# Optimization experiments

Hardware: AMD Instinct MI355X
Metric: run time of the kernel (lower is better)

Reference implementation:

```python
import jax, jax.numpy as jnp
import numpy as np

H = 256; NH = 4; DH = H // NH
NT, NS, NV = 4096, 2048, 1024
E1, E2, E3 = 65536, 16384, 32768
LN_EPS = 1e-5


def setup_inputs() -> dict:
    key = jax.random.key(0)
    ks = jax.random.split(key, 40)
    def nrm(i, shape):
        return jax.random.normal(ks[i], shape, jnp.float32) * 0.05
    inp = {
        "x_term": jax.random.normal(ks[0], (NT, H), jnp.float32),
        "x_symbol": jax.random.normal(ks[1], (NS, H), jnp.float32),
        "x_var": jax.random.normal(ks[2], (NV, H), jnp.float32),
        "ha_src": jax.random.randint(ks[3], (E1,), 0, NT),
        "ha_dst": jax.random.randint(ks[4], (E1,), 0, NT),
        "so_src": jax.random.randint(ks[5], (E2,), 0, NT),
        "so_dst": jax.random.randint(ks[6], (E2,), 0, NS),
        "vo_src": jax.random.randint(ks[7], (E3,), 0, NV),
        "vo_dst": jax.random.randint(ks[8], (E3,), 0, NT),
        # SAGEConv params for the 4 term-destination relations
        "Wl_rha": nrm(9, (H, H)),  "bl_rha": nrm(10, (H,)), "Wr_rha": nrm(11, (H, H)),
        "Wl_ha":  nrm(12, (H, H)), "bl_ha":  nrm(13, (H,)), "Wr_ha":  nrm(14, (H, H)),
        "Wl_rsym": nrm(15, (H, H)), "bl_rsym": nrm(16, (H,)), "Wr_rsym": nrm(17, (H, H)),
        "Wl_var": nrm(18, (H, H)), "bl_var": nrm(19, (H,)), "Wr_var": nrm(20, (H, H)),
        "ln_g": jnp.ones((H,), jnp.float32),
        "ln_b": jnp.zeros((H,), jnp.float32),
        "in_proj_w": nrm(21, (3 * H, H)),
        "in_proj_b": nrm(22, (3 * H,)),
        "out_proj_w": nrm(23, (H, H)),
        "out_proj_b": nrm(24, (H,)),
        "post_w": nrm(25, (H, H)),
        "post_b": nrm(26, (H,)),
    }
    return inp


def _sage(x_src, x_dst, src, dst, Wl, bl, Wr, num_dst):
    # PyG SAGEConv: lin_l(mean_j x_src[j]) + lin_r(x_dst)
    msg = x_src[src]                                            # [E, H] gather
    s = jax.ops.segment_sum(msg, dst, num_segments=num_dst)     # [N_dst, H] scatter-add
    cnt = jax.ops.segment_sum(jnp.ones((src.shape[0],), x_src.dtype), dst,
                              num_segments=num_dst)
    agg = s / jnp.maximum(cnt, 1.0)[:, None]
    return agg @ Wl.T + bl + x_dst @ Wr.T


def _layernorm(x, g, b):
    mu = jnp.mean(x, axis=-1, keepdims=True)
    var = jnp.mean(jnp.square(x - mu), axis=-1, keepdims=True)
    return (x - mu) * jax.lax.rsqrt(var + LN_EPS) * g + b


def _mha(x, in_w, in_b, out_w, out_b):
    # torch MultiheadAttention (eval, batch=1, self-attention)
    qkv = x @ in_w.T + in_b                       # [N, 3H]
    q, k, v = jnp.split(qkv, 3, axis=-1)
    def heads(t):
        return t.reshape(-1, NH, DH).transpose(1, 0, 2)  # [NH, N, DH]
    q, k, v = heads(q), heads(k), heads(v)
    scores = jnp.einsum("hqd,hkd->hqk", q, k) / np.sqrt(DH).astype(np.float32)
    a = jax.nn.softmax(scores, axis=-1)
    o = jnp.einsum("hqk,hkd->hqd", a, v)          # [NH, N, DH]
    o = o.transpose(1, 0, 2).reshape(-1, H)
    return o @ out_w.T + out_b


def reference(x_term, x_symbol, x_var,
              ha_src, ha_dst, so_src, so_dst, vo_src, vo_dst,
              Wl_rha, bl_rha, Wr_rha, Wl_ha, bl_ha, Wr_ha,
              Wl_rsym, bl_rsym, Wr_rsym, Wl_var, bl_var, Wr_var,
              ln_g, ln_b, in_proj_w, in_proj_b, out_proj_w, out_proj_b,
              post_w, post_b):
    nt = x_term.shape[0]
    # HeteroConv(aggr='sum') over the 4 relations whose destination is 'term'
    conv_term = (
        _sage(x_term, x_term, ha_dst, ha_src, Wl_rha, bl_rha, Wr_rha, nt)    # rev_has_arg
        + _sage(x_term, x_term, ha_src, ha_dst, Wl_ha, bl_ha, Wr_ha, nt)     # has_arg
        + _sage(x_symbol, x_term, so_dst, so_src, Wl_rsym, bl_rsym, Wr_rsym, nt)  # rev_symbol_of
        + _sage(x_var, x_term, vo_src, vo_dst, Wl_var, bl_var, Wr_var, nt)   # var_occurrence
    )
    term_out = _layernorm(conv_term + x_term, ln_g, ln_b)  # dropout is identity in eval
    attn_out = _mha(term_out, in_proj_w, in_proj_b, out_proj_w, out_proj_b)
    post = jax.nn.relu(attn_out @ post_w.T + post_b)
    term_final = post + term_out
    return term_final
```

## Files before the change

kernel.cpp:

```cpp
#include <hip/hip_runtime.h>
#include <hip/hip_bf16.h>

#define H 256
#define NT 4096
#define NHEAD 4
#define E1 65536
#define E2 16384
#define E3 32768
#define TOTE (2 * E1 + E2 + E3)
#define LN_EPS 1e-5f
#define SPLIT 4

typedef __hip_bfloat16 bf16;
typedef short bf16x8 __attribute__((ext_vector_type(8)));
typedef float f32x4 __attribute__((ext_vector_type(4)));

__device__ __forceinline__ float b2f(bf16 v) { return __bfloat162float(v); }
__device__ __forceinline__ float u2f(unsigned short u) {
    unsigned int x = ((unsigned int)u) << 16;
    return __uint_as_float(x);
}
__device__ __forceinline__ unsigned short f2u(float f) {
    bf16 h = __float2bfloat16(f);
    unsigned short v;
    __builtin_memcpy(&v, &h, 2);
    return v;
}
__device__ __forceinline__ float ldin(const void* p, size_t i, bool isbf) {
    return isbf ? b2f(((const bf16*)p)[i]) : ((const float*)p)[i];
}

__global__ __launch_bounds__(256) void k_init(float4* cnt4, int n4,
                                              const unsigned int* __restrict__ lng,
                                              unsigned int* __restrict__ flag) {
    int i = blockIdx.x * 256 + threadIdx.x;
    if (i == 0) *flag = (lng[0] == 0x3F803F80u) ? 1u : 0u;
    int stride = gridDim.x * 256;
    float4 z = make_float4(0.f, 0.f, 0.f, 0.f);
    for (; i < n4; i += stride) cnt4[i] = z;
}

__global__ __launch_bounds__(256) void k_count4(const int* __restrict__ s0, const int* __restrict__ s1,
                                                const int* __restrict__ s2, const int* __restrict__ s3,
                                                int* __restrict__ cnt) {
    int i = blockIdx.x * 256 + threadIdx.x;
    int r, e;
    if (i < E1) { r = 0; e = i; }
    else if (i < 2 * E1) { r = 1; e = i - E1; }
    else if (i < 2 * E1 + E2) { r = 2; e = i - 2 * E1; }
    else if (i < TOTE) { r = 3; e = i - 2 * E1 - E2; }
    else return;
    const int* s = (r == 0) ? s0 : (r == 1) ? s1 : (r == 2) ? s2 : s3;
    atomicAdd(&cnt[r * NT + s[e]], 1);
}

__global__ __launch_bounds__(256) void k_scan(const int* __restrict__ cnt, int* __restrict__ offs,
                                              int* __restrict__ cursor) {
    __shared__ int tot[256];
    int t = threadIdx.x, r = blockIdx.x;
    const int* c = cnt + r * NT;
    int* o = offs + r * (NT + 1);
    int* cur = cursor + r * NT;
    int base = t * 16;
    int local[16];
    int sum = 0;
#pragma unroll
    for (int j = 0; j < 16; j++) { local[j] = c[base + j]; sum += local[j]; }
    tot[t] = sum;
    __syncthreads();
    if (t == 0) {
        int run = 0;
        for (int i = 0; i < 256; i++) { int v = tot[i]; tot[i] = run; run += v; }
        o[NT] = run;
    }
    __syncthreads();
    int run = tot[t];
#pragma unroll
    for (int j = 0; j < 16; j++) { o[base + j] = run; cur[base + j] = run; run += local[j]; }
}

__global__ __launch_bounds__(256) void k_fill(const int* __restrict__ s0, const int* __restrict__ s1,
                                              const int* __restrict__ s2, const int* __restrict__ s3,
                                              const int* __restrict__ g0, const int* __restrict__ g1,
                                              const int* __restrict__ g2, const int* __restrict__ g3,
                                              int* __restrict__ cursor, int* __restrict__ csr) {
    int i = blockIdx.x * 256 + threadIdx.x;
    int r, e, rb;
    if (i < E1) { r = 0; e = i; rb = 0; }
    else if (i < 2 * E1) { r = 1; e = i - E1; rb = E1; }
    else if (i < 2 * E1 + E2) { r = 2; e = i - 2 * E1; rb = 2 * E1; }
    else if (i < TOTE) { r = 3; e = i - 2 * E1 - E2; rb = 2 * E1 + E2; }
    else return;
    const int* s = (r == 0) ? s0 : (r == 1) ? s1 : (r == 2) ? s2 : s3;
    const int* g = (r == 0) ? g0 : (r == 1) ? g1 : (r == 2) ? g2 : g3;
    int d = s[e];
    int pos = atomicAdd(&cursor[r * NT + d], 1);
    csr[rb + pos] = g[e];
}

__global__ __launch_bounds__(256) void k_gatherA(
    const void* __restrict__ x0, const void* __restrict__ x1,
    const void* __restrict__ x2, const void* __restrict__ x3,
    const int* __restrict__ offs, const int* __restrict__ csr,
    bf16* __restrict__ aggs, const unsigned int* __restrict__ flag) {
    int y = blockIdx.y;
    int i = blockIdx.x * 4 + (threadIdx.x >> 6);
    int lane = threadIdx.x & 63;
    bool isbf = (*flag != 0u);
    const void* x = (y == 0) ? x0 : (y == 1) ? x1 : (y == 2) ? x2 : x3;
    static const int rbase[4] = {0, E1, 2 * E1, 2 * E1 + E2};
    const int* o = offs + y * (NT + 1);
    const int* cs = csr + rbase[y];
    int b = o[i], e = o[i + 1];
    float ax = 0.f, ay = 0.f, az = 0.f, aw = 0.f;
    if (isbf) {
        for (int j = b; j < e; j++) {
            int s = cs[j];
            ushort4 u = *(const ushort4*)((const unsigned short*)x + (size_t)s * H + lane * 4);
            ax += u2f(u.x); ay += u2f(u.y); az += u2f(u.z); aw += u2f(u.w);
        }
    } else {
        for (int j = b; j < e; j++) {
            int s = cs[j];
            float4 v = *(const float4*)((const float*)x + (size_t)s * H + lane * 4);
            ax += v.x; ay += v.y; az += v.z; aw += v.w;
        }
    }
    float inv = 1.0f / fmaxf((float)(e - b), 1.0f);
    *(ushort4*)((unsigned short*)aggs + ((size_t)y * NT + i) * H + lane * 4) =
        make_ushort4(f2u(ax * inv), f2u(ay * inv), f2u(az * inv), f2u(aw * inv));
}

__global__ __launch_bounds__(256) void k_prepB(
    const void* __restrict__ Wl0, const void* __restrict__ Wl1,
    const void* __restrict__ Wl2, const void* __restrict__ Wl3,
    const void* __restrict__ Wr0, const void* __restrict__ Wr1,
    const void* __restrict__ Wr2, const void* __restrict__ Wr3,
    const void* __restrict__ b0, const void* __restrict__ b1,
    const void* __restrict__ b2, const void* __restrict__ b3,
    bf16* __restrict__ Bcat, float* __restrict__ bsum, const unsigned int* __restrict__ flag) {
    int idx = blockIdx.x * 256 + threadIdx.x;
    bool isbf = (*flag != 0u);
    int n = idx / 1280, k = idx % 1280;
    float v;
    if (k < 1024) {
        const void* W = (k < 256) ? Wl0 : (k < 512) ? Wl1 : (k < 768) ? Wl2 : Wl3;
        v = ldin(W, (size_t)n * 256 + (k & 255), isbf);
    } else {
        size_t o = (size_t)n * 256 + (k - 1024);
        v = ldin(Wr0, o, isbf) + ldin(Wr1, o, isbf) + ldin(Wr2, o, isbf) + ldin(Wr3, o, isbf);
    }
    ((unsigned short*)Bcat)[idx] = f2u(v);
    if (idx < 256)
        bsum[idx] = ldin(b0, idx, isbf) + ldin(b1, idx, isbf) + ldin(b2, idx, isbf) + ldin(b3, idx, isbf);
}

__global__ __launch_bounds__(256) void k_convln(
    const bf16* __restrict__ aggs, const bf16* __restrict__ Bcat, const float* __restrict__ bsum,
    const void* __restrict__ xt, const void* __restrict__ gw, const void* __restrict__ gb,
    bf16* __restrict__ term, const unsigned int* __restrict__ flag) {
    __shared__ unsigned short Asm[4 * 16 * 8];
    __shared__ unsigned short Bsm[4 * 256 * 8];
    __shared__ float redS[4][16];
    const bool isbf = (*flag != 0u);
    const int tid = threadIdx.x;
    const int w = tid >> 6, lane = tid & 63;
    const int col = lane & 15, quad = lane >> 4;
    const int m0 = blockIdx.x * 16;
    const int srow = tid & 63, skq = tid >> 6;

    f32x4 acc[4];
#pragma unroll
    for (int dt = 0; dt < 4; dt++) acc[dt] = (f32x4){0.f, 0.f, 0.f, 0.f};

    bf16x8 areg;
    bf16x8 breg[4];
    auto loadA = [&](int k0) {
        if (tid < 64) {
            int row = tid & 15, akq = tid >> 4;
            int k = k0 + akq * 8;
            if (k < 1024) {
                areg = *(const bf16x8*)((const unsigned short*)aggs +
                                        ((size_t)(k >> 8) * NT + m0 + row) * 256 + (k & 255));
            } else {
#pragma unroll
                for (int j = 0; j < 8; j++)
                    areg[j] = (short)f2u(ldin(xt, (size_t)(m0 + row) * 256 + (k - 1024) + j, isbf));
            }
        }
    };
    auto loadB = [&](int k0) {
#pragma unroll
        for (int t = 0; t < 4; t++)
            breg[t] = *(const bf16x8*)((const unsigned short*)Bcat +
                                       (size_t)(t * 64 + srow) * 1280 + k0 + skq * 8);
    };

    loadA(0);
    loadB(0);
    for (int k0 = 0; k0 < 1280; k0 += 32) {
        __syncthreads();
        if (tid < 64) *(bf16x8*)&Asm[tid * 8] = areg;
#pragma unroll
        for (int t = 0; t < 4; t++)
            *(bf16x8*)&Bsm[(skq * 256 + t * 64 + srow) * 8] = breg[t];
        __syncthreads();
        if (k0 + 32 < 1280) { loadA(k0 + 32); loadB(k0 + 32); }
        bf16x8 a = *(const bf16x8*)&Asm[(quad * 16 + col) * 8];
#pragma unroll
        for (int dt = 0; dt < 4; dt++) {
            bf16x8 b = *(const bf16x8*)&Bsm[(quad * 256 + w * 64 + dt * 16 + col) * 8];
            acc[dt] = __builtin_amdgcn_mfma_f32_16x16x32_bf16(a, b, acc[dt], 0, 0, 0);
        }
    }

#pragma unroll
    for (int dt = 0; dt < 4; dt++) {
        int n = w * 64 + dt * 16 + col;
        float bsv = bsum[n];
#pragma unroll
        for (int r = 0; r < 4; r++) {
            int m = m0 + quad * 4 + r;
            acc[dt][r] += bsv + ldin(xt, (size_t)m * 256 + n, isbf);
        }
    }
    float mu[4], rs_[4];
#pragma unroll
    for (int r = 0; r < 4; r++) {
        float s = acc[0][r] + acc[1][r] + acc[2][r] + acc[3][r];
#pragma unroll
        for (int mk = 1; mk <= 8; mk <<= 1) s += __shfl_xor(s, mk);
        if (col == 0) redS[w][quad * 4 + r] = s;
    }
    __syncthreads();
#pragma unroll
    for (int r = 0; r < 4; r++) {
        int m = quad * 4 + r;
        mu[r] = (redS[0][m] + redS[1][m] + redS[2][m] + redS[3][m]) * (1.0f / 256.0f);
    }
    __syncthreads();
#pragma unroll
    for (int r = 0; r < 4; r++) {
        float s2 = 0.f;
#pragma unroll
        for (int dt = 0; dt < 4; dt++) {
            float d = acc[dt][r] - mu[r];
            s2 += d * d;
        }
#pragma unroll
        for (int mk = 1; mk <= 8; mk <<= 1) s2 += __shfl_xor(s2, mk);
        if (col == 0) redS[w][quad * 4 + r] = s2;
    }
    __syncthreads();
#pragma unroll
    for (int r = 0; r < 4; r++) {
        int m = quad * 4 + r;
        float var = (redS[0][m] + redS[1][m] + redS[2][m] + redS[3][m]) * (1.0f / 256.0f);
        rs_[r] = rsqrtf(var + LN_EPS);
    }
#pragma unroll
    for (int dt = 0; dt < 4; dt++) {
        int n = w * 64 + dt * 16 + col;
        float gv = ldin(gw, n, isbf), bv = ldin(gb, n, isbf);
#pragma unroll
        for (int r = 0; r < 4; r++) {
            int m = m0 + quad * 4 + r;
            term[(size_t)m * 256 + n] = __float2bfloat16((acc[dt][r] - mu[r]) * rs_[r] * gv + bv);
        }
    }
}

template <int AMODE, int EPI>
__global__ __launch_bounds__(256) void k_gemm(
    const void* __restrict__ A, const void* __restrict__ A2, const float* __restrict__ ml,
    const void* __restrict__ B, const void* __restrict__ bias,
    const bf16* __restrict__ resid, void* __restrict__ outp,
    int M, int N, int K, const unsigned int* __restrict__ flag) {
    __shared__ unsigned short Asm[4 * 64 * 8];
    __shared__ unsigned short Bsm[4 * 64 * 8];
    const bool isbf = (*flag != 0u);
    const int tid = threadIdx.x;
    const int w = tid >> 6, lane = tid & 63;
    const int col = lane & 15, quad = lane >> 4;
    const int m0 = blockIdx.x * 64, n0 = blockIdx.y * 64;
    const int srow = tid & 63, skq = tid >> 6;
    const int am = m0 + srow;

    f32x4 acc[4];
#pragma unroll
    for (int dt = 0; dt < 4; dt++) acc[dt] = (f32x4){0.f, 0.f, 0.f, 0.f};

    bf16x8 areg, breg;
    auto loadA = [&](int k0) {
        int k = k0 + skq * 8;
        if (AMODE == 0) {
            areg = *(const bf16x8*)((const unsigned short*)A + (size_t)am * K + k);
        } else {
            int h = k >> 6;
            float l0 = ml[(size_t)(0 * NHEAD + h) * NT + am];
            float l1 = ml[(size_t)(1 * NHEAD + h) * NT + am];
            float l2 = ml[(size_t)(2 * NHEAD + h) * NT + am];
            float l3 = ml[(size_t)(3 * NHEAD + h) * NT + am];
            float iw = 1.0f / (l0 + l1 + l2 + l3);
            bf16x8 o0 = *(const bf16x8*)((const unsigned short*)A + (size_t)am * H + k);
            bf16x8 o1 = *(const bf16x8*)((const unsigned short*)A + ((size_t)NT + am) * H + k);
            bf16x8 o2 = *(const bf16x8*)((const unsigned short*)A2 + (size_t)am * H + k);
            bf16x8 o3 = *(const bf16x8*)((const unsigned short*)A2 + ((size_t)NT + am) * H + k);
#pragma unroll
            for (int j = 0; j < 8; j++)
                areg[j] = (short)f2u((l0 * u2f((unsigned short)o0[j]) + l1 * u2f((unsigned short)o1[j]) +
                                      l2 * u2f((unsigned short)o2[j]) + l3 * u2f((unsigned short)o3[j])) * iw);
        }
    };
    auto loadB = [&](int k0) {
        size_t bi = (size_t)(n0 + srow) * K + k0 + skq * 8;
        if (isbf) {
            breg = *(const bf16x8*)((const unsigned short*)B + bi);
        } else {
#pragma unroll
            for (int j = 0; j < 8; j++) breg[j] = (short)f2u(((const float*)B)[bi + j]);
        }
    };

    loadA(0);
    loadB(0);
    for (int k0 = 0; k0 < K; k0 += 32) {
        __syncthreads();
        *(bf16x8*)&Asm[tid * 8] = areg;
        *(bf16x8*)&Bsm[tid * 8] = breg;
        __syncthreads();
        if (k0 + 32 < K) { loadA(k0 + 32); loadB(k0 + 32); }
        bf16x8 a = *(const bf16x8*)&Asm[(quad * 64 + w * 16 + col) * 8];
#pragma unroll
        for (int dt = 0; dt < 4; dt++) {
            bf16x8 b = *(const bf16x8*)&Bsm[(quad * 64 + dt * 16 + col) * 8];
            acc[dt] = __builtin_amdgcn_mfma_f32_16x16x32_bf16(a, b, acc[dt], 0, 0, 0);
        }
    }
#pragma unroll
    for (int dt = 0; dt < 4; dt++) {
        int n = n0 + dt * 16 + col;
        float bv = ldin(bias, n, isbf);
#pragma unroll
        for (int r = 0; r < 4; r++) {
            int m = m0 + w * 16 + quad * 4 + r;
            float v = acc[dt][r] + bv;
            size_t off = (size_t)m * N + n;
            if (EPI == 2) {
                v = fmaxf(v, 0.f);
                v += b2f(resid[off]);
                ((float*)outp)[off] = v;
            } else {
                ((bf16*)outp)[off] = __float2bfloat16(v);
            }
        }
    }
}

__global__ __launch_bounds__(256) void k_attn(const bf16* __restrict__ qkv,
                                              bf16* __restrict__ opart01,
                                              bf16* __restrict__ opart23,
                                              float* __restrict__ ml) {
    __shared__ unsigned short Ksm[8 * 64 * 8];
    __shared__ unsigned short Vt[8 * 64 * 8];
    __shared__ unsigned short Psm[4][1024];
    const int h = blockIdx.y, sp = blockIdx.z;
    const int q0 = blockIdx.x * 64;
    const int tid = threadIdx.x;
    const int w = tid >> 6, lane = tid & 63;
    const int col = lane & 15, quad = lane >> 4;
    const unsigned short* qk = (const unsigned short*)qkv;

    bf16x8 aQ[2];
#pragma unroll
    for (int ch = 0; ch < 2; ch++)
        aQ[ch] = *(const bf16x8*)(qk + (size_t)(q0 + w * 16 + col) * 768 + h * 64 + ch * 32 + quad * 8);

    f32x4 O[4];
#pragma unroll
    for (int dt = 0; dt < 4; dt++) O[dt] = (f32x4){0.f, 0.f, 0.f, 0.f};
    float lsum[4] = {0.f, 0.f, 0.f, 0.f};

    const int kbeg = sp * (NT / SPLIT), kend = kbeg + NT / SPLIT;
    const float SC = 0.125f * 1.44269504f;

    bf16x8 kreg[2], vreg[2];
    auto loadKV = [&](int kb) {
#pragma unroll
        for (int it = 0; it < 2; it++) {
            int cid = tid + it * 256;
            int kkey = cid & 63, dhq = cid >> 6;
            kreg[it] = *(const bf16x8*)(qk + (size_t)(kb + kkey) * 768 + 256 + h * 64 + dhq * 8);
            int vkey = cid >> 3, d8 = cid & 7;
            vreg[it] = *(const bf16x8*)(qk + (size_t)(kb + vkey) * 768 + 512 + h * 64 + d8 * 8);
        }
    };
    loadKV(kbeg);

    for (int kb = kbeg; kb < kend; kb += 64) {
        __syncthreads();
#pragma unroll
        for (int it = 0; it < 2; it++) {
            int cid = tid + it * 256;
            *(bf16x8*)&Ksm[cid * 8] = kreg[it];
            int vkey = cid >> 3, d8 = cid & 7;
            int kh = (vkey >> 3) * 512 + (vkey & 7);
#pragma unroll
            for (int jj = 0; jj < 8; jj++) {
                int j = (jj + lane) & 7;
                Vt[kh + (d8 * 8 + j) * 8] = (unsigned short)vreg[it][j];
            }
        }
        __syncthreads();
        if (kb + 64 < kend) loadKV(kb + 64);

        f32x4 c[4];
#pragma unroll
        for (int dt = 0; dt < 4; dt++) {
            c[dt] = (f32x4){0.f, 0.f, 0.f, 0.f};
#pragma unroll
            for (int ch = 0; ch < 2; ch++) {
                bf16x8 b = *(const bf16x8*)&Ksm[((ch * 4 + quad) * 64 + dt * 16 + col) * 8];
                c[dt] = __builtin_amdgcn_mfma_f32_16x16x32_bf16(aQ[ch], b, c[dt], 0, 0, 0);
            }
#pragma unroll
            for (int r = 0; r < 4; r++) {
                float p = exp2f(c[dt][r] * SC);
                c[dt][r] = p;
                lsum[r] += p;
            }
        }
#pragma unroll
        for (int dt = 0; dt < 4; dt++) {
            int k = dt * 16 + col;
#pragma unroll
            for (int r = 0; r < 4; r++) {
                int ql = quad * 4 + r;
                Psm[w][(k >> 3) * 128 + ql * 8 + (k & 7)] = f2u(c[dt][r]);
            }
        }
        bf16x8 aP[2];
#pragma unroll
        for (int kc = 0; kc < 2; kc++)
            aP[kc] = *(const bf16x8*)&Psm[w][(kc * 4 + quad) * 128 + col * 8];
#pragma unroll
        for (int dt = 0; dt < 4; dt++) {
#pragma unroll
            for (int kc = 0; kc < 2; kc++) {
                bf16x8 b = *(const bf16x8*)&Vt[((kc * 4 + quad) * 64 + dt * 16 + col) * 8];
                O[dt] = __builtin_amdgcn_mfma_f32_16x16x32_bf16(aP[kc], b, O[dt], 0, 0, 0);
            }
        }
    }
    float l[4];
#pragma unroll
    for (int r = 0; r < 4; r++) {
        float s = lsum[r];
#pragma unroll
        for (int mk = 1; mk <= 8; mk <<= 1) s += __shfl_xor(s, mk);
        l[r] = s;
    }
    bf16* ob = (sp < 2) ? (opart01 + (size_t)sp * NT * H) : (opart23 + (size_t)(sp - 2) * NT * H);
#pragma unroll
    for (int dt = 0; dt < 4; dt++) {
#pragma unroll
        for (int r = 0; r < 4; r++) {
            int q = q0 + w * 16 + quad * 4 + r;
            ob[(size_t)q * H + h * 64 + dt * 16 + col] = __float2bfloat16(O[dt][r] / l[r]);
        }
    }
    if (col == 0) {
#pragma unroll
        for (int r = 0; r < 4; r++) {
            int q = q0 + w * 16 + quad * 4 + r;
            ml[((size_t)sp * NHEAD + h) * NT + q] = l[r];
        }
    }
}

extern "C" void kernel_launch(void* const* d_in, const int* in_sizes, int n_in,
                              void* d_out, int out_size, void* d_ws, size_t ws_size,
                              hipStream_t stream) {
    const void* x_term   = d_in[0];
    const void* x_symbol = d_in[1];
    const void* x_var    = d_in[2];
    const int* ha_src = (const int*)d_in[3];
    const int* ha_dst = (const int*)d_in[4];
    const int* so_src = (const int*)d_in[5];
    const int* so_dst = (const int*)d_in[6];
    const int* vo_src = (const int*)d_in[7];
    const int* vo_dst = (const int*)d_in[8];
    const void* Wl[4]  = {d_in[9],  d_in[12], d_in[15], d_in[18]};
    const void* blv[4] = {d_in[10], d_in[13], d_in[16], d_in[19]};
    const void* Wr[4]  = {d_in[11], d_in[14], d_in[17], d_in[20]};
    const void* ln_g = d_in[21];
    const void* ln_b = d_in[22];
    const void* in_w = d_in[23];
    const void* in_b = d_in[24];
    const void* out_w = d_in[25];
    const void* out_b = d_in[26];
    const void* post_w = d_in[27];
    const void* post_b = d_in[28];

    char* ws = (char*)d_ws;
    unsigned int* flag = (unsigned int*)ws;
    char* csrbase = ws + 256;
    int* cnt    = (int*)csrbase;
    int* offs   = (int*)(csrbase + 65536);
    int* cursor = (int*)(csrbase + 132096);
    int* csr    = (int*)(csrbase + 197632);
    bf16*  Bcat = (bf16*)csrbase;
    float* bsum = (float*)(csrbase + 655360);
    float* ml   = (float*)csrbase;
    bf16* aggs  = (bf16*)(ws + (1 << 20));
    bf16* term  = (bf16*)(ws + (1 << 20) + 8388608);
    bf16* opart23 = (bf16*)(ws + (1 << 20) + 10485760);
    bf16* qkvp  = aggs;
    bf16* proj  = aggs;
    bf16* opart01 = (bf16*)d_out;

    k_init<<<16, 256, 0, stream>>>((float4*)cnt, 4 * NT / 4, (const unsigned int*)ln_g, flag);
    k_count4<<<(TOTE + 255) / 256, 256, 0, stream>>>(ha_src, ha_dst, so_src, vo_dst, cnt);
    k_scan<<<4, 256, 0, stream>>>(cnt, offs, cursor);
    k_fill<<<(TOTE + 255) / 256, 256, 0, stream>>>(ha_src, ha_dst, so_src, vo_dst,
                                                   ha_dst, ha_src, so_dst, vo_src, cursor, csr);
    k_gatherA<<<dim3(NT / 4, 4), 256, 0, stream>>>(x_term, x_term, x_symbol, x_var,
                                                   offs, csr, aggs, flag);
    k_prepB<<<(256 * 1280) / 256, 256, 0, stream>>>(Wl[0], Wl[1], Wl[2], Wl[3],
                                                    Wr[0], Wr[1], Wr[2], Wr[3],
                                                    blv[0], blv[1], blv[2], blv[3],
                                                    Bcat, bsum, flag);

    k_convln<<<256, 256, 0, stream>>>(aggs, Bcat, bsum, x_term, ln_g, ln_b, term, flag);

    k_gemm<0, 0><<<dim3(64, 12), 256, 0, stream>>>(
        term, nullptr, nullptr, in_w, in_b, nullptr, qkvp, NT, 768, 256, flag);

    k_attn<<<dim3(64, NHEAD, SPLIT), 256, 0, stream>>>(qkvp, opart01, opart23, ml);

    k_gemm<1, 0><<<dim3(64, 4), 256, 0, stream>>>(
        opart01, opart23, ml, out_w, out_b, nullptr, proj, NT, 256, 256, flag);

    k_gemm<0, 2><<<dim3(64, 4), 256, 0, stream>>>(
        proj, nullptr, nullptr, post_w, post_b, term, d_out, NT, 256, 256, flag);

    (void)in_sizes; (void)n_in; (void)out_size; (void)ws_size;
}
```

Measured before the change: 309.1 us.

## Write V transposed from QKV GEMM and drop attention LDS staging; fuse weight prep

The QKV projection epilogue now writes Q and K into a 512-wide buffer and writes V transposed into a separate buffer. The attention kernel can then load K and V MFMA operands straight from global memory into registers, removing the shared-memory staging, the in-LDS V transpose and the per-block barriers. Separately, the k_prepB weight-concatenation kernel is removed and convln reads and sums the SAGE weights and biases inline, saving a launch. The trade-off is repeated global or L2 loads per wave in attention, and redundant Wr summation across convln blocks.

```diff
diff --git a/kernel.cpp b/kernel.cpp
--- a/kernel.cpp
+++ b/kernel.cpp
@@ -131,32 +131,14 @@
         make_ushort4(f2u(ax * inv), f2u(ay * inv), f2u(az * inv), f2u(aw * inv));
 }
 
-__global__ __launch_bounds__(256) void k_prepB(
+__global__ __launch_bounds__(256) void k_convln(
+    const bf16* __restrict__ aggs,
     const void* __restrict__ Wl0, const void* __restrict__ Wl1,
     const void* __restrict__ Wl2, const void* __restrict__ Wl3,
     const void* __restrict__ Wr0, const void* __restrict__ Wr1,
     const void* __restrict__ Wr2, const void* __restrict__ Wr3,
-    const void* __restrict__ b0, const void* __restrict__ b1,
-    const void* __restrict__ b2, const void* __restrict__ b3,
-    bf16* __restrict__ Bcat, float* __restrict__ bsum, const unsigned int* __restrict__ flag) {
-    int idx = blockIdx.x * 256 + threadIdx.x;
-    bool isbf = (*flag != 0u);
-    int n = idx / 1280, k = idx % 1280;
-    float v;
-    if (k < 1024) {
-        const void* W = (k < 256) ? Wl0 : (k < 512) ? Wl1 : (k < 768) ? Wl2 : Wl3;
-        v = ldin(W, (size_t)n * 256 + (k & 255), isbf);
-    } else {
-        size_t o = (size_t)n * 256 + (k - 1024);
-        v = ldin(Wr0, o, isbf) + ldin(Wr1, o, isbf) + ldin(Wr2, o, isbf) + ldin(Wr3, o, isbf);
-    }
-    ((unsigned short*)Bcat)[idx] = f2u(v);
-    if (idx < 256)
-        bsum[idx] = ldin(b0, idx, isbf) + ldin(b1, idx, isbf) + ldin(b2, idx, isbf) + ldin(b3, idx, isbf);
-}
-
-__global__ __launch_bounds__(256) void k_convln(
-    const bf16* __restrict__ aggs, const bf16* __restrict__ Bcat, const float* __restrict__ bsum,
+    const void* __restrict__ bl0, const void* __restrict__ bl1,
+    const void* __restrict__ bl2, const void* __restrict__ bl3,
     const void* __restrict__ xt, const void* __restrict__ gw, const void* __restrict__ gb,
     bf16* __restrict__ term, const unsigned int* __restrict__ flag) {
     __shared__ unsigned short Asm[4 * 16 * 8];
@@ -190,10 +172,29 @@
         }
     };
     auto loadB = [&](int k0) {
-#pragma unroll
-        for (int t = 0; t < 4; t++)
-            breg[t] = *(const bf16x8*)((const unsigned short*)Bcat +
-                                       (size_t)(t * 64 + srow) * 1280 + k0 + skq * 8);
+        int k = k0 + skq * 8;
+#pragma unroll
+        for (int t = 0; t < 4; t++) {
+            int n = t * 64 + srow;
+            bf16x8 s;
+            if (k < 1024) {
+                const void* W = (k < 256) ? Wl0 : (k < 512) ? Wl1 : (k < 768) ? Wl2 : Wl3;
+                size_t o = (size_t)n * 256 + (k & 255);
+                if (isbf) {
+                    s = *(const bf16x8*)((const unsigned short*)W + o);
+                } else {
+#pragma unroll
+                    for (int j = 0; j < 8; j++) s[j] = (short)f2u(((const float*)W)[o + j]);
+                }
+            } else {
+                size_t o = (size_t)n * 256 + (k - 1024);
+#pragma unroll
+                for (int j = 0; j < 8; j++)
+                    s[j] = (short)f2u(ldin(Wr0, o + j, isbf) + ldin(Wr1, o + j, isbf) +
+                                      ldin(Wr2, o + j, isbf) + ldin(Wr3, o + j, isbf));
+            }
+            breg[t] = s;
+        }
     };
 
     loadA(0);
@@ -217,7 +218,7 @@
 #pragma unroll
     for (int dt = 0; dt < 4; dt++) {
         int n = w * 64 + dt * 16 + col;
-        float bsv = bsum[n];
+        float bsv = ldin(bl0, n, isbf) + ldin(bl1, n, isbf) + ldin(bl2, n, isbf) + ldin(bl3, n, isbf);
 #pragma unroll
         for (int r = 0; r < 4; r++) {
             int m = m0 + quad * 4 + r;
@@ -274,7 +275,7 @@
 __global__ __launch_bounds__(256) void k_gemm(
     const void* __restrict__ A, const void* __restrict__ A2, const float* __restrict__ ml,
     const void* __restrict__ B, const void* __restrict__ bias,
-    const bf16* __restrict__ resid, void* __restrict__ outp,
+    const bf16* __restrict__ resid, bf16* __restrict__ vt, void* __restrict__ outp,
     int M, int N, int K, const unsigned int* __restrict__ flag) {
     __shared__ unsigned short Asm[4 * 64 * 8];
     __shared__ unsigned short Bsm[4 * 64 * 8];
@@ -341,40 +342,49 @@
     for (int dt = 0; dt < 4; dt++) {
         int n = n0 + dt * 16 + col;
         float bv = ldin(bias, n, isbf);
+        if (EPI == 3 && n0 >= 512) {
+            int m = m0 + w * 16 + quad * 4;
+            *(ushort4*)((unsigned short*)vt + (size_t)(n - 512) * NT + m) =
+                make_ushort4(f2u(acc[dt][0] + bv), f2u(acc[dt][1] + bv),
+                             f2u(acc[dt][2] + bv), f2u(acc[dt][3] + bv));
+            continue;
+        }
 #pragma unroll
         for (int r = 0; r < 4; r++) {
             int m = m0 + w * 16 + quad * 4 + r;
             float v = acc[dt][r] + bv;
-            size_t off = (size_t)m * N + n;
-            if (EPI == 2) {
+            if (EPI == 3) {
+                ((bf16*)outp)[(size_t)m * 512 + n] = __float2bfloat16(v);
+            } else if (EPI == 2) {
+                size_t off = (size_t)m * N + n;
                 v = fmaxf(v, 0.f);
                 v += b2f(resid[off]);
                 ((float*)outp)[off] = v;
             } else {
-                ((bf16*)outp)[off] = __float2bfloat16(v);
+                ((bf16*)outp)[(size_t)m * N + n] = __float2bfloat16(v);
             }
         }
     }
 }
 
-__global__ __launch_bounds__(256) void k_attn(const bf16* __restrict__ qkv,
+__global__ __launch_bounds__(256) void k_attn(const bf16* __restrict__ qkvQK,
+                                              const bf16* __restrict__ vt,
                                               bf16* __restrict__ opart01,
                                               bf16* __restrict__ opart23,
                                               float* __restrict__ ml) {
-    __shared__ unsigned short Ksm[8 * 64 * 8];
-    __shared__ unsigned short Vt[8 * 64 * 8];
     __shared__ unsigned short Psm[4][1024];
     const int h = blockIdx.y, sp = blockIdx.z;
     const int q0 = blockIdx.x * 64;
     const int tid = threadIdx.x;
     const int w = tid >> 6, lane = tid & 63;
     const int col = lane & 15, quad = lane >> 4;
-    const unsigned short* qk = (const unsigned short*)qkv;
+    const unsigned short* qk = (const unsigned short*)qkvQK;
+    const unsigned short* vp = (const unsigned short*)vt;
 
     bf16x8 aQ[2];
 #pragma unroll
     for (int ch = 0; ch < 2; ch++)
-        aQ[ch] = *(const bf16x8*)(qk + (size_t)(q0 + w * 16 + col) * 768 + h * 64 + ch * 32 + quad * 8);
+        aQ[ch] = *(const bf16x8*)(qk + (size_t)(q0 + w * 16 + col) * 512 + h * 64 + ch * 32 + quad * 8);
 
     f32x4 O[4];
 #pragma unroll
@@ -384,45 +394,29 @@
     const int kbeg = sp * (NT / SPLIT), kend = kbeg + NT / SPLIT;
     const float SC = 0.125f * 1.44269504f;
 
-    bf16x8 kreg[2], vreg[2];
-    auto loadKV = [&](int kb) {
-#pragma unroll
-        for (int it = 0; it < 2; it++) {
-            int cid = tid + it * 256;
-            int kkey = cid & 63, dhq = cid >> 6;
-            kreg[it] = *(const bf16x8*)(qk + (size_t)(kb + kkey) * 768 + 256 + h * 64 + dhq * 8);
-            int vkey = cid >> 3, d8 = cid & 7;
-            vreg[it] = *(const bf16x8*)(qk + (size_t)(kb + vkey) * 768 + 512 + h * 64 + d8 * 8);
-        }
-    };
-    loadKV(kbeg);
-
     for (int kb = kbeg; kb < kend; kb += 64) {
-        __syncthreads();
-#pragma unroll
-        for (int it = 0; it < 2; it++) {
-            int cid = tid + it * 256;
-            *(bf16x8*)&Ksm[cid * 8] = kreg[it];
-            int vkey = cid >> 3, d8 = cid & 7;
-            int kh = (vkey >> 3) * 512 + (vkey & 7);
-#pragma unroll
-            for (int jj = 0; jj < 8; jj++) {
-                int j = (jj + lane) & 7;
-                Vt[kh + (d8 * 8 + j) * 8] = (unsigned short)vreg[it][j];
-            }
-        }
-        __syncthreads();
-        if (kb + 64 < kend) loadKV(kb + 64);
+        bf16x8 bK[4][2];
+#pragma unroll
+        for (int dt = 0; dt < 4; dt++)
+#pragma unroll
+            for (int ch = 0; ch < 2; ch++)
+                bK[dt][ch] = *(const bf16x8*)(qk + (size_t)(kb + dt * 16 + col) * 512 + 256 +
+                                              h * 64 + ch * 32 + quad * 8);
+        bf16x8 bV[4][2];
+#pragma unroll
+        for (int dt = 0; dt < 4; dt++)
+#pragma unroll
+            for (int kc = 0; kc < 2; kc++)
+                bV[dt][kc] = *(const bf16x8*)(vp + (size_t)(h * 64 + dt * 16 + col) * NT +
+                                              kb + kc * 32 + quad * 8);
 
         f32x4 c[4];
 #pragma unroll
         for (int dt = 0; dt < 4; dt++) {
             c[dt] = (f32x4){0.f, 0.f, 0.f, 0.f};
 #pragma unroll
-            for (int ch = 0; ch < 2; ch++) {
-                bf16x8 b = *(const bf16x8*)&Ksm[((ch * 4 + quad) * 64 + dt * 16 + col) * 8];
-                c[dt] = __builtin_amdgcn_mfma_f32_16x16x32_bf16(aQ[ch], b, c[dt], 0, 0, 0);
-            }
+            for (int ch = 0; ch < 2; ch++)
+                c[dt] = __builtin_amdgcn_mfma_f32_16x16x32_bf16(aQ[ch], bK[dt][ch], c[dt], 0, 0, 0);
 #pragma unroll
             for (int r = 0; r < 4; r++) {
                 float p = exp2f(c[dt][r] * SC);
@@ -444,13 +438,10 @@
         for (int kc = 0; kc < 2; kc++)
             aP[kc] = *(const bf16x8*)&Psm[w][(kc * 4 + quad) * 128 + col * 8];
 #pragma unroll
-        for (int dt = 0; dt < 4; dt++) {
-#pragma unroll
-            for (int kc = 0; kc < 2; kc++) {
-                bf16x8 b = *(const bf16x8*)&Vt[((kc * 4 + quad) * 64 + dt * 16 + col) * 8];
-                O[dt] = __builtin_amdgcn_mfma_f32_16x16x32_bf16(aP[kc], b, O[dt], 0, 0, 0);
-            }
-        }
+        for (int dt = 0; dt < 4; dt++)
+#pragma unroll
+            for (int kc = 0; kc < 2; kc++)
+                O[dt] = __builtin_amdgcn_mfma_f32_16x16x32_bf16(aP[kc], bV[dt][kc], O[dt], 0, 0, 0);
     }
     float l[4];
 #pragma unroll
@@ -509,13 +500,12 @@
     int* offs   = (int*)(csrbase + 65536);
     int* cursor = (int*)(csrbase + 132096);
     int* csr    = (int*)(csrbase + 197632);
-    bf16*  Bcat = (bf16*)csrbase;
-    float* bsum = (float*)(csrbase + 655360);
     float* ml   = (float*)csrbase;
     bf16* aggs  = (bf16*)(ws + (1 << 20));
     bf16* term  = (bf16*)(ws + (1 << 20) + 8388608);
     bf16* opart23 = (bf16*)(ws + (1 << 20) + 10485760);
-    bf16* qkvp  = aggs;
+    bf16* qkvQK = aggs;
+    bf16* vt    = (bf16*)((char*)aggs + 4194304);
     bf16* proj  = aggs;
     bf16* opart01 = (bf16*)d_out;
 
@@ -526,23 +516,22 @@
                                                    ha_dst, ha_src, so_dst, vo_src, cursor, csr);
     k_gatherA<<<dim3(NT / 4, 4), 256, 0, stream>>>(x_term, x_term, x_symbol, x_var,
                                                    offs, csr, aggs, flag);
-    k_prepB<<<(256 * 1280) / 256, 256, 0, stream>>>(Wl[0], Wl[1], Wl[2], Wl[3],
-                                                    Wr[0], Wr[1], Wr[2], Wr[3],
-                                                    blv[0], blv[1], blv[2], blv[3],
-                                                    Bcat, bsum, flag);
-
-    k_convln<<<256, 256, 0, stream>>>(aggs, Bcat, bsum, x_term, ln_g, ln_b, term, flag);
-
-    k_gemm<0, 0><<<dim3(64, 12), 256, 0, stream>>>(
-        term, nullptr, nullptr, in_w, in_b, nullptr, qkvp, NT, 768, 256, flag);
-
-    k_attn<<<dim3(64, NHEAD, SPLIT), 256, 0, stream>>>(qkvp, opart01, opart23, ml);
+
+    k_convln<<<256, 256, 0, stream>>>(aggs, Wl[0], Wl[1], Wl[2], Wl[3],
+                                      Wr[0], Wr[1], Wr[2], Wr[3],
+                                      blv[0], blv[1], blv[2], blv[3],
+                                      x_term, ln_g, ln_b, term, flag);
+
+    k_gemm<0, 3><<<dim3(64, 12), 256, 0, stream>>>(
+        term, nullptr, nullptr, in_w, in_b, nullptr, vt, qkvQK, NT, 768, 256, flag);
+
+    k_attn<<<dim3(64, NHEAD, SPLIT), 256, 0, stream>>>(qkvQK, vt, opart01, opart23, ml);
 
     k_gemm<1, 0><<<dim3(64, 4), 256, 0, stream>>>(
-        opart01, opart23, ml, out_w, out_b, nullptr, proj, NT, 256, 256, flag);
+        opart01, opart23, ml, out_w, out_b, nullptr, nullptr, proj, NT, 256, 256, flag);
 
     k_gemm<0, 2><<<dim3(64, 4), 256, 0, stream>>>(
-        proj, nullptr, nullptr, post_w, post_b, term, d_out, NT, 256, 256, flag);
+        proj, nullptr, nullptr, post_w, post_b, term, nullptr, d_out, NT, 256, 256, flag);
 
     (void)in_sizes; (void)n_in; (void)out_size; (void)ws_size;
 }
```

After: 619.3 us. 2x slower.
